# Performance work log

Hardware: AMD Instinct MI355X
Metric: run time of the kernel (lower is better)

The kernel has to match this reference:

```python
import jax, jax.numpy as jnp
import numpy as np

EMB = 768
HID = 3072
HID2 = 2 * HID
NE = 8
K = 2
B, N = 8, 2048


def setup_inputs() -> dict:
    key = jax.random.key(0)
    ks = jax.random.split(key, 9)
    s = lambda *d: 1.0 / np.sqrt(d[-2])  # ~ torch Linear init scale
    inp = {
        'x': jax.random.normal(ks[0], (B, N, EMB), dtype=jnp.float32),
        'Wg': jax.random.normal(ks[1], (EMB, NE), dtype=jnp.float32) * (1.0 / np.sqrt(EMB)),
        'bg': jnp.zeros((NE,), dtype=jnp.float32),
        'W1': jax.random.normal(ks[2], (NE, EMB, HID), dtype=jnp.float32) * (1.0 / np.sqrt(EMB)),
        'b1': jnp.zeros((NE, HID), dtype=jnp.float32),
        'W2': jax.random.normal(ks[3], (NE, HID, HID2), dtype=jnp.float32) * (1.0 / np.sqrt(HID)),
        'b2': jnp.zeros((NE, HID2), dtype=jnp.float32),
        'W3': jax.random.normal(ks[4], (NE, HID2, EMB), dtype=jnp.float32) * (1.0 / np.sqrt(HID2)),
        'b3': jnp.zeros((NE, EMB), dtype=jnp.float32),
    }
    return inp


def _gelu(x):
    return jax.nn.gelu(x, approximate=False)  # torch nn.GELU default (erf)


def reference(x, Wg, bg, W1, b1, W2, b2, W3, b3):
    # gating: top-k over expert scores, softmax over the k selected logits
    scores = x @ Wg + bg                     # [B,N,NE]
    topk_vals, topk_idx = jax.lax.top_k(scores, K)   # [B,N,K]
    gates = jax.nn.softmax(topk_vals, axis=-1)       # [B,N,K]
    # dense combine weights: c[b,n,e] = sum_i gates[...,i] * (idx[...,i]==e)
    onehot = jax.nn.one_hot(topk_idx, NE, dtype=x.dtype)  # [B,N,K,NE]
    comb = jnp.einsum('bnk,bnke->bne', gates, onehot)     # [B,N,NE]
    out = jnp.zeros_like(x)
    for e in range(NE):  # small fixed expert loop
        h = _gelu(x @ W1[e] + b1[e])       # [B,N,HID]
        h = _gelu(h @ W2[e] + b2[e])       # [B,N,HID2]
        y = h @ W3[e] + b3[e]              # [B,N,EMB]
        out = out + comb[..., e:e + 1] * y
    return out
```

## Files before the change

### kernel.cpp

```cpp
#include <hip/hip_runtime.h>
#include <hip/hip_bf16.h>

#define EMB 768
#define HID 3072
#define HID2 6144
#define NE 8
#define TOK 16384
#define SLOTS 32768
#define SLACK 256
#define MAXTILES 136

typedef __attribute__((ext_vector_type(8))) short bf16x8;
typedef __attribute__((ext_vector_type(4))) float f32x4;

__device__ __forceinline__ unsigned short bfbits(float f) {
  __hip_bfloat16 h = __float2bfloat16(f);
  return __builtin_bit_cast(unsigned short, h);
}


__global__ void k_init(int* counts, int* fill) {
  if (threadIdx.x < NE) { counts[threadIdx.x] = 0; fill[threadIdx.x] = 0; }
}

__global__ __launch_bounds__(256) void k_gating(
    const float* __restrict__ x, const float* __restrict__ Wg,
    const float* __restrict__ bg, int* __restrict__ eidx,
    float* __restrict__ gates)
{
  const int wave = threadIdx.x >> 6, lane = threadIdx.x & 63;
  const int t = blockIdx.x * 4 + wave;
  const float* xr = x + (size_t)t * EMB;
  float p[NE];
#pragma unroll
  for (int e = 0; e < NE; ++e) p[e] = 0.f;
  for (int k = lane; k < EMB; k += 64) {
    const float xv = xr[k];
    const float* wr = Wg + (size_t)k * NE;
#pragma unroll
    for (int e = 0; e < NE; ++e) p[e] += xv * wr[e];
  }
#pragma unroll
  for (int e = 0; e < NE; ++e) {
#pragma unroll
    for (int o = 32; o > 0; o >>= 1) p[e] += __shfl_xor(p[e], o);
    p[e] += bg[e];
  }
  float v0 = -1e30f, v1 = -1e30f; int i0 = 0, i1 = 0;
#pragma unroll
  for (int e = 0; e < NE; ++e) {
    const float v = p[e];
    if (v > v0)      { v1 = v0; i1 = i0; v0 = v; i0 = e; }
    else if (v > v1) { v1 = v;  i1 = e; }
  }
  const float ex = expf(v1 - v0);
  const float g0 = 1.f / (1.f + ex);
  const float g1 = 1.f - g0;
  if (lane == 0) {
    eidx[2*t] = i0; eidx[2*t+1] = i1;
    gates[2*t] = g0; gates[2*t+1] = g1;
  }
}

__global__ __launch_bounds__(256) void k_count(const int* __restrict__ eidx,
                                               int* __restrict__ counts)
{
  __shared__ int bins[NE];
  if (threadIdx.x < NE) bins[threadIdx.x] = 0;
  __syncthreads();
  const int base = blockIdx.x * 512 + threadIdx.x * 2;
  atomicAdd(&bins[eidx[base]], 1);
  atomicAdd(&bins[eidx[base + 1]], 1);
  __syncthreads();
  if (threadIdx.x < NE) atomicAdd(&counts[threadIdx.x], bins[threadIdx.x]);
}

__global__ void k_offsets(const int* __restrict__ counts, int* __restrict__ offsets,
                          int* __restrict__ tmap)
{
  offsets[0] = 0;
  int idx = 0;
  for (int e = 0; e < NE; ++e) {
    offsets[e+1] = offsets[e] + counts[e];
    const int nt = (counts[e] + 255) >> 8;
    for (int i = 0; i < nt; ++i) tmap[idx++] = (e << 16) | i;
  }
  for (; idx < MAXTILES; ++idx) tmap[idx] = -1;
}

__global__ __launch_bounds__(256) void k_route(
    const int* __restrict__ eidx, int* __restrict__ fill,
    const int* __restrict__ offsets, int* __restrict__ route_tok,
    float* __restrict__ gate_slot, int* __restrict__ tok_k,
    const float* __restrict__ gates)
{
  __shared__ int bins[NE], base[NE];
  const int tid = threadIdx.x;
  if (tid < NE) bins[tid] = 0;
  __syncthreads();
  const int t = blockIdx.x * 256 + tid;
  int e0 = eidx[2*t], e1 = eidx[2*t+1];
  int lp0 = atomicAdd(&bins[e0], 1);
  int lp1 = atomicAdd(&bins[e1], 1);
  __syncthreads();
  if (tid < NE) base[tid] = atomicAdd(&fill[tid], bins[tid]);
  __syncthreads();
  const int s0 = offsets[e0] + base[e0] + lp0;
  const int s1 = offsets[e1] + base[e1] + lp1;
  route_tok[s0] = t;          route_tok[s1] = t;
  gate_slot[s0] = gates[2*t]; gate_slot[s1] = gates[2*t+1];
  tok_k[s0] = 2*t;            tok_k[s1] = 2*t + 1;
}

__global__ __launch_bounds__(256) void k_gather(
    const float* __restrict__ x, const int* __restrict__ route_tok,
    __hip_bfloat16* __restrict__ xg)
{
  const int w = threadIdx.x >> 6, lane = threadIdx.x & 63;
  const int s = blockIdx.x * 4 + w;
  const int t = route_tok[s];
  const float4* src = (const float4*)(x + (size_t)t * EMB);
  unsigned short* dst = (unsigned short*)xg + (size_t)s * EMB;
#pragma unroll
  for (int i = 0; i < 3; ++i) {
    const float4 v = src[lane + 64 * i];
    ushort4 u;
    u.x = bfbits(v.x); u.y = bfbits(v.y); u.z = bfbits(v.z); u.w = bfbits(v.w);
    *(ushort4*)(dst + (lane + 64 * i) * 4) = u;
  }
}

#define NT1 (NE * (HID  / 64) * (EMB  / 64))
#define NT2 (NE * (HID2 / 64) * (HID  / 64))
#define NT3 (NE * (EMB  / 64) * (HID2 / 64))

typedef __attribute__((ext_vector_type(8))) unsigned short u16x8;

__global__ __launch_bounds__(256) void k_transpose_all(
    const float* __restrict__ W1, const float* __restrict__ W2,
    const float* __restrict__ W3, __hip_bfloat16* __restrict__ Wb1,
    __hip_bfloat16* __restrict__ Wb2, __hip_bfloat16* __restrict__ Wb3)
{
  __shared__ float tile[64][65];
  int bid = blockIdx.x;
  const float* W; __hip_bfloat16* Wt; int K, N;
  if (bid < NT1)              { W = W1; Wt = Wb1; K = EMB;  N = HID;  }
  else if (bid < NT1 + NT2)   { W = W2; Wt = Wb2; K = HID;  N = HID2; bid -= NT1; }
  else                        { W = W3; Wt = Wb3; K = HID2; N = EMB;  bid -= NT1 + NT2; }
  const int ntn = N >> 6, ntk = K >> 6;
  const int e  = bid / (ntn * ntk);
  const int rem = bid - e * (ntn * ntk);
  const int k0 = (rem / ntn) << 6;
  const int n0 = (rem % ntn) << 6;

  const float* Wp = W + (size_t)e * K * N;
  __hip_bfloat16* Wtp = Wt + (size_t)e * K * N;
  const int tx = threadIdx.x, ty = threadIdx.y;

  const int q = tx & 15, rsub = tx >> 4;
#pragma unroll
  for (int it = 0; it < 4; ++it) {
    const int r = it * 16 + ty * 2 + rsub;
    const float4 v = *(const float4*)(Wp + (size_t)(k0 + r) * N + n0 + 4 * q);
    tile[r][4 * q]     = v.x;
    tile[r][4 * q + 1] = v.y;
    tile[r][4 * q + 2] = v.z;
    tile[r][4 * q + 3] = v.w;
  }
  __syncthreads();
  const int q8 = tx & 7, r8 = tx >> 3;
#pragma unroll
  for (int it = 0; it < 2; ++it) {
    const int n = it * 32 + ty * 4 + r8;
    u16x8 u;
#pragma unroll
    for (int j = 0; j < 8; ++j) u[j] = bfbits(tile[8 * q8 + j][n]);
    *(u16x8*)((unsigned short*)Wtp + (size_t)(n0 + n) * K + k0 + 8 * q8) = u;
  }
}


#define BARRIER() asm volatile("s_barrier" ::: "memory")

template<bool GELU, bool OUTBF, bool SCATTER>
__global__ __launch_bounds__(512) void ffn_gemm8(
    const __hip_bfloat16* __restrict__ A,
    const __hip_bfloat16* __restrict__ Bt,
    const float* __restrict__ bias,
    void* __restrict__ Cout,
    const int* __restrict__ counts,
    const int* __restrict__ offsets,
    const int* __restrict__ tmap,
    const float* __restrict__ gate_slot,
    const int* __restrict__ tok_k,
    int K, int N)
{
  const int me = tmap[blockIdx.y];
  if (me < 0) return;
  const int e  = me >> 16;
  const int m0 = (me & 0xffff) << 8;
  const int cnt = counts[e];
  const int seg = offsets[e];
  const int n0 = blockIdx.x * 256;

  __shared__ char lds[131072];

  const int tid = threadIdx.x;
  const int wave = tid >> 6, lane = tid & 63;
  const int wm = wave >> 2, wn = wave & 3;

  const size_t KB = (size_t)K * 2;
  const char* Ag = (const char*)(A + (size_t)(seg + m0) * K);
  const char* Bg = (const char*)(Bt + (size_t)e * N * K + (size_t)n0 * K);

  const int s_r  = tid >> 2;
  const int s_cb = ((tid & 3) * 16) ^ (((s_r >> 1) & 3) << 4);

  auto stage_half = [&](const char* gbase, int kbyte, int ldsoff) {
    const char* s = gbase + (size_t)s_r * KB + kbyte + s_cb;
    __builtin_amdgcn_global_load_lds(
        (const __attribute__((address_space(1))) void*)s,
        (__attribute__((address_space(3))) void*)(lds + ldsoff + tid * 16), 16, 0, 0);
    __builtin_amdgcn_global_load_lds(
        (const __attribute__((address_space(1))) void*)(s + 128 * KB),
        (__attribute__((address_space(3))) void*)(lds + ldsoff + 8192 + tid * 16), 16, 0, 0);
  };

  const int fr    = lane & 15;
  const int coff  = ((lane >> 4) * 16) ^ (((fr >> 1) & 3) << 4);
  const int aoff0 = (wm * 128 + fr) * 64 + coff;
  const int boff0 = 32768 + (wn * 64 + fr) * 64 + coff;

  f32x4 acc[8][4];
#pragma unroll
  for (int i = 0; i < 8; ++i)
#pragma unroll
    for (int j = 0; j < 4; ++j)
      acc[i][j] = (f32x4){0.f, 0.f, 0.f, 0.f};

  const int KT = K >> 6;

  stage_half(Ag, 0, 0);
  stage_half(Bg, 0, 32768);
  stage_half(Ag, 64, 16384);
  stage_half(Bg, 64, 49152);
  asm volatile("s_waitcnt vmcnt(4)" ::: "memory");
  BARRIER();

  bf16x8 a[8], b[4];

  for (int kt = 0; kt < KT; ++kt) {
    const int sb  = (kt & 1) * 65536;
    const int sl1 = sb ^ 65536;
    const int kbN = (kt + 1 < KT ? kt + 1 : KT - 1) * 128;

#pragma unroll
    for (int m = 0; m < 8; ++m)
      a[m] = *(const bf16x8*)(lds + sb + aoff0 + m * 1024);
#pragma unroll
    for (int n = 0; n < 4; ++n)
      b[n] = *(const bf16x8*)(lds + sb + boff0 + n * 1024);
    stage_half(Ag, kbN, sl1);
    stage_half(Bg, kbN, sl1 + 32768);
#pragma unroll
    for (int m = 0; m < 8; ++m)
#pragma unroll
      for (int n = 0; n < 4; ++n)
        acc[m][n] = __builtin_amdgcn_mfma_f32_16x16x32_bf16(a[m], b[n], acc[m][n], 0, 0, 0);
    asm volatile("s_waitcnt vmcnt(4)" ::: "memory");
    BARRIER();

#pragma unroll
    for (int m = 0; m < 8; ++m)
      a[m] = *(const bf16x8*)(lds + sb + 16384 + aoff0 + m * 1024);
#pragma unroll
    for (int n = 0; n < 4; ++n)
      b[n] = *(const bf16x8*)(lds + sb + 16384 + boff0 + n * 1024);
    stage_half(Ag, kbN + 64, sl1 + 16384);
    stage_half(Bg, kbN + 64, sl1 + 49152);
#pragma unroll
    for (int m = 0; m < 8; ++m)
#pragma unroll
      for (int n = 0; n < 4; ++n)
        acc[m][n] = __builtin_amdgcn_mfma_f32_16x16x32_bf16(a[m], b[n], acc[m][n], 0, 0, 0);
    asm volatile("s_waitcnt vmcnt(4)" ::: "memory");
    BARRIER();
  }

#pragma unroll
  for (int mf = 0; mf < 8; ++mf) {
#pragma unroll
    for (int r2 = 0; r2 < 4; ++r2) {
      const int gm = m0 + wm * 128 + mf * 16 + (lane >> 4) * 4 + r2;
      if (gm >= cnt) continue;
      if (SCATTER) {
        const int s = seg + gm;
        const float g = gate_slot[s];
        const int tk = tok_k[s];
        float* dst = (float*)Cout + ((size_t)(tk & 1) * TOK + (size_t)(tk >> 1)) * EMB;
#pragma unroll
        for (int nf = 0; nf < 4; ++nf) {
          const int gcol = n0 + wn * 64 + nf * 16 + fr;
          dst[gcol] = g * (acc[mf][nf][r2] + bias[(size_t)e * N + gcol]);
        }
      } else {
#pragma unroll
        for (int nf = 0; nf < 4; ++nf) {
          const int gcol = n0 + wn * 64 + nf * 16 + fr;
          float v = acc[mf][nf][r2] + bias[(size_t)e * N + gcol];
          if (GELU) v = 0.5f * v * (1.0f + erff(v * 0.70710678118654752f));
          if (OUTBF)
            ((__hip_bfloat16*)Cout)[(size_t)(seg + gm) * N + gcol] = __float2bfloat16(v);
          else
            ((float*)Cout)[(size_t)(seg + gm) * N + gcol] = v;
        }
      }
    }
  }
}

__global__ __launch_bounds__(256) void k_combine2(const float* __restrict__ ybuf2,
                                                  float* __restrict__ out)
{
  const size_t total = (size_t)TOK * EMB / 4;
  for (size_t i = blockIdx.x * 256 + threadIdx.x; i < total; i += (size_t)gridDim.x * 256) {
    const float4 a = ((const float4*)ybuf2)[i];
    const float4 b = ((const float4*)(ybuf2 + (size_t)TOK * EMB))[i];
    float4 o;
    o.x = a.x + b.x; o.y = a.y + b.y; o.z = a.z + b.z; o.w = a.w + b.w;
    ((float4*)out)[i] = o;
  }
}


extern "C" void kernel_launch(void* const* d_in, const int* in_sizes, int n_in,
                              void* d_out, int out_size, void* d_ws, size_t ws_size,
                              hipStream_t stream)
{
  const float* x  = (const float*)d_in[0];
  const float* Wg = (const float*)d_in[1];
  const float* bg = (const float*)d_in[2];
  const float* W1 = (const float*)d_in[3];
  const float* b1 = (const float*)d_in[4];
  const float* W2 = (const float*)d_in[5];
  const float* b2 = (const float*)d_in[6];
  const float* W3 = (const float*)d_in[7];
  const float* b3 = (const float*)d_in[8];
  float* out = (float*)d_out;

  char* ws = (char*)d_ws;
  size_t off = 0;
  auto alloc = [&](size_t bytes) -> void* {
    void* p = ws + off;
    off = (off + bytes + 255) & ~(size_t)255;
    return p;
  };

  int*   counts    = (int*)alloc(NE * 4);
  int*   fill      = (int*)alloc(NE * 4);
  int*   offsets   = (int*)alloc((NE + 1) * 4);
  int*   tmap      = (int*)alloc(MAXTILES * 4);
  int*   eidx      = (int*)alloc((size_t)TOK * 2 * 4);
  float* gates     = (float*)alloc((size_t)TOK * 2 * 4);
  int*   route_tok = (int*)alloc((size_t)SLOTS * 4);
  float* gate_slot = (float*)alloc((size_t)(SLOTS + SLACK) * 4);
  int*   tok_k     = (int*)alloc((size_t)(SLOTS + SLACK) * 4);
  __hip_bfloat16* Wb1 = (__hip_bfloat16*)alloc((size_t)NE * EMB  * HID  * 2);
  __hip_bfloat16* Wb2 = (__hip_bfloat16*)alloc((size_t)NE * HID  * HID2 * 2);
  __hip_bfloat16* Wb3 = (__hip_bfloat16*)alloc((size_t)NE * HID2 * EMB  * 2);
  __hip_bfloat16* xg  = (__hip_bfloat16*)alloc((size_t)(SLOTS + SLACK) * EMB  * 2);
  __hip_bfloat16* h1  = (__hip_bfloat16*)alloc((size_t)(SLOTS + SLACK) * HID  * 2);
  __hip_bfloat16* h2  = (__hip_bfloat16*)alloc((size_t)(SLOTS + SLACK) * HID2 * 2);
  float*          ybuf2 = (float*)alloc((size_t)2 * TOK * EMB * 4);
  (void)ws_size; (void)in_sizes; (void)n_in; (void)out_size;

  k_init<<<1, 64, 0, stream>>>(counts, fill);
  k_gating<<<TOK / 4, 256, 0, stream>>>(x, Wg, bg, eidx, gates);
  k_count<<<SLOTS / 512, 256, 0, stream>>>(eidx, counts);
  k_offsets<<<1, 1, 0, stream>>>(counts, offsets, tmap);
  k_route<<<TOK / 256, 256, 0, stream>>>(eidx, fill, offsets, route_tok,
                                         gate_slot, tok_k, gates);
  k_gather<<<SLOTS / 4, 256, 0, stream>>>(x, route_tok, xg);

  k_transpose_all<<<NT1 + NT2 + NT3, dim3(32, 8), 0, stream>>>(W1, W2, W3, Wb1, Wb2, Wb3);

  ffn_gemm8<true,  true,  false><<<dim3(HID  / 256, MAXTILES), 512, 0, stream>>>(
      xg, Wb1, b1, h1, counts, offsets, tmap, nullptr, nullptr, EMB,  HID);
  ffn_gemm8<true,  true,  false><<<dim3(HID2 / 256, MAXTILES), 512, 0, stream>>>(
      h1, Wb2, b2, h2, counts, offsets, tmap, nullptr, nullptr, HID,  HID2);
  ffn_gemm8<false, false, true ><<<dim3(EMB  / 256, MAXTILES), 512, 0, stream>>>(
      h2, Wb3, b3, ybuf2, counts, offsets, tmap, gate_slot, tok_k, HID2, EMB);

  k_combine2<<<2048, 256, 0, stream>>>(ybuf2, out);
}
```

Before: 2.572 ms.

## Software-pipeline LDS reads with MFMA using ping-pong register fragments

Restructures the GEMM main loop into a four-slot LDS ring of K=32 phases. Each phase reads the next fragments into alternate register sets (even/odd) while the MFMAs for the previous phase run, and partial lgkmcnt waits plus sched_barrier fences control the interleaving. The intent is to hide LDS read latency behind matrix math, where the old loop waited on the reads before issuing each MFMA block. The cost is twice the fragment registers, which raises register pressure, and a tail that re-stages the last phase redundantly.

```diff
diff --git a/kernel.cpp b/kernel.cpp
--- a/kernel.cpp
+++ b/kernel.cpp
@@ -181,6 +181,8 @@
 
 
 #define BARRIER() asm volatile("s_barrier" ::: "memory")
+#define LGKM(n) { asm volatile("s_waitcnt lgkmcnt(" #n ")" ::: "memory"); __builtin_amdgcn_sched_barrier(0); }
+#define VMC(n)  { asm volatile("s_waitcnt vmcnt(" #n ")" ::: "memory"); __builtin_amdgcn_sched_barrier(0); }
 
 template<bool GELU, bool OUTBF, bool SCATTER>
 __global__ __launch_bounds__(512) void ffn_gemm8(
@@ -216,20 +218,29 @@
   const int s_r  = tid >> 2;
   const int s_cb = ((tid & 3) * 16) ^ (((s_r >> 1) & 3) << 4);
 
-  auto stage_half = [&](const char* gbase, int kbyte, int ldsoff) {
-    const char* s = gbase + (size_t)s_r * KB + kbyte + s_cb;
+  auto S = [&](int x) {
+    const int ub = (x & 3) * 32768;
+    const int kbyte = x * 64;
+    const char* sa = Ag + (size_t)s_r * KB + kbyte + s_cb;
+    const char* sb = Bg + (size_t)s_r * KB + kbyte + s_cb;
     __builtin_amdgcn_global_load_lds(
-        (const __attribute__((address_space(1))) void*)s,
-        (__attribute__((address_space(3))) void*)(lds + ldsoff + tid * 16), 16, 0, 0);
+        (const __attribute__((address_space(1))) void*)sa,
+        (__attribute__((address_space(3))) void*)(lds + ub + tid * 16), 16, 0, 0);
     __builtin_amdgcn_global_load_lds(
-        (const __attribute__((address_space(1))) void*)(s + 128 * KB),
-        (__attribute__((address_space(3))) void*)(lds + ldsoff + 8192 + tid * 16), 16, 0, 0);
+        (const __attribute__((address_space(1))) void*)(sa + 128 * KB),
+        (__attribute__((address_space(3))) void*)(lds + ub + 8192 + tid * 16), 16, 0, 0);
+    __builtin_amdgcn_global_load_lds(
+        (const __attribute__((address_space(1))) void*)sb,
+        (__attribute__((address_space(3))) void*)(lds + ub + 16384 + tid * 16), 16, 0, 0);
+    __builtin_amdgcn_global_load_lds(
+        (const __attribute__((address_space(1))) void*)(sb + 128 * KB),
+        (__attribute__((address_space(3))) void*)(lds + ub + 16384 + 8192 + tid * 16), 16, 0, 0);
   };
 
   const int fr    = lane & 15;
   const int coff  = ((lane >> 4) * 16) ^ (((fr >> 1) & 3) << 4);
   const int aoff0 = (wm * 128 + fr) * 64 + coff;
-  const int boff0 = 32768 + (wn * 64 + fr) * 64 + coff;
+  const int boff0 = 16384 + (wn * 64 + fr) * 64 + coff;
 
   f32x4 acc[8][4];
 #pragma unroll
@@ -238,54 +249,63 @@
     for (int j = 0; j < 4; ++j)
       acc[i][j] = (f32x4){0.f, 0.f, 0.f, 0.f};
 
-  const int KT = K >> 6;
-
-  stage_half(Ag, 0, 0);
-  stage_half(Bg, 0, 32768);
-  stage_half(Ag, 64, 16384);
-  stage_half(Bg, 64, 49152);
-  asm volatile("s_waitcnt vmcnt(4)" ::: "memory");
+  const int NPH = K >> 5;
+
+  bf16x8 aE[8], bE[4], aO[8], bO[4];
+
+#define RD(x, as, bs) {                                             \
+    const char* ub_ = lds + ((x) & 3) * 32768;                      \
+    _Pragma("unroll")                                               \
+    for (int m_ = 0; m_ < 8; ++m_)                                  \
+      as[m_] = *(const bf16x8*)(ub_ + aoff0 + m_ * 1024);           \
+    _Pragma("unroll")                                               \
+    for (int n_ = 0; n_ < 4; ++n_)                                  \
+      bs[n_] = *(const bf16x8*)(ub_ + boff0 + n_ * 1024); }
+
+#define MM(as, bs) {                                                \
+    _Pragma("unroll")                                               \
+    for (int m_ = 0; m_ < 8; ++m_)                                  \
+      _Pragma("unroll")                                             \
+      for (int n_ = 0; n_ < 4; ++n_)                                \
+        acc[m_][n_] = __builtin_amdgcn_mfma_f32_16x16x32_bf16(      \
+            as[m_], bs[n_], acc[m_][n_], 0, 0, 0); }
+
+  S(0); S(1);
+  VMC(4);
   BARRIER();
 
-  bf16x8 a[8], b[4];
-
-  for (int kt = 0; kt < KT; ++kt) {
-    const int sb  = (kt & 1) * 65536;
-    const int sl1 = sb ^ 65536;
-    const int kbN = (kt + 1 < KT ? kt + 1 : KT - 1) * 128;
-
-#pragma unroll
-    for (int m = 0; m < 8; ++m)
-      a[m] = *(const bf16x8*)(lds + sb + aoff0 + m * 1024);
-#pragma unroll
-    for (int n = 0; n < 4; ++n)
-      b[n] = *(const bf16x8*)(lds + sb + boff0 + n * 1024);
-    stage_half(Ag, kbN, sl1);
-    stage_half(Bg, kbN, sl1 + 32768);
-#pragma unroll
-    for (int m = 0; m < 8; ++m)
-#pragma unroll
-      for (int n = 0; n < 4; ++n)
-        acc[m][n] = __builtin_amdgcn_mfma_f32_16x16x32_bf16(a[m], b[n], acc[m][n], 0, 0, 0);
-    asm volatile("s_waitcnt vmcnt(4)" ::: "memory");
+  RD(0, aE, bE);
+  S(2);
+  VMC(4);
+  BARRIER();
+
+  RD(1, aO, bO);
+  S(3);
+  LGKM(12);
+  MM(aE, bE);
+  VMC(4);
+  BARRIER();
+
+  for (int p = 2; p < NPH; p += 2) {
+    RD(p, aE, bE);
+    S(p + 2 < NPH ? p + 2 : NPH - 1);
+    LGKM(12);
+    MM(aO, bO);
+    VMC(4);
     BARRIER();
-
-#pragma unroll
-    for (int m = 0; m < 8; ++m)
-      a[m] = *(const bf16x8*)(lds + sb + 16384 + aoff0 + m * 1024);
-#pragma unroll
-    for (int n = 0; n < 4; ++n)
-      b[n] = *(const bf16x8*)(lds + sb + 16384 + boff0 + n * 1024);
-    stage_half(Ag, kbN + 64, sl1 + 16384);
-    stage_half(Bg, kbN + 64, sl1 + 49152);
-#pragma unroll
-    for (int m = 0; m < 8; ++m)
-#pragma unroll
-      for (int n = 0; n < 4; ++n)
-        acc[m][n] = __builtin_amdgcn_mfma_f32_16x16x32_bf16(a[m], b[n], acc[m][n], 0, 0, 0);
-    asm volatile("s_waitcnt vmcnt(4)" ::: "memory");
+    RD(p + 1, aO, bO);
+    S(p + 3 < NPH ? p + 3 : NPH - 1);
+    LGKM(12);
+    MM(aE, bE);
+    VMC(4);
     BARRIER();
   }
+
+  LGKM(0);
+  MM(aO, bO);
+
+#undef RD
+#undef MM
 
 #pragma unroll
   for (int mf = 0; mf < 8; ++mf) {
```

Result: faster. 2.434 ms (-5.3%).
